# Performance work log

Measured on AMD Instinct MI355X. Metric: run time of the kernel, lower is better.

Reference implementation:

```python
import jax, jax.numpy as jnp
import numpy as np

B, N, F, T = 32, 1024, 64, 24


def setup_inputs() -> dict:
    key = jax.random.key(0)
    k = jax.random.split(key, 6)
    x = jax.random.normal(k[0], (B, N, F, T), dtype=jnp.float32)
    W1 = jax.random.normal(k[1], (T,), dtype=jnp.float32) * 0.1
    W2 = jax.random.normal(k[2], (F, T), dtype=jnp.float32) * 0.1
    W3 = jax.random.normal(k[3], (F,), dtype=jnp.float32) * 0.1
    b_s = jax.random.normal(k[4], (1, N, N), dtype=jnp.float32) * 0.02
    V_s = jax.random.normal(k[5], (N, N), dtype=jnp.float32) * 0.02
    return {"x": x, "W1": W1, "W2": W2, "W3": W3, "b_s": b_s, "V_s": V_s}


def reference(x, W1, W2, W3, b_s, V_s):
    # lhs = (x @ W1) @ W2 : (B,N,F,T)@(T,) -> (B,N,F) ; @(F,T) -> (B,N,T)
    lhs = jnp.einsum('bnft,t->bnf', x, W1) @ W2
    # rhs = (x^T @ W3) permuted : (B,N,T,F)@(F,) -> (B,N,T) -> (B,T,N)
    rhs = jnp.einsum('bnft,f->btn', x, W3)
    # batch_dot: (B,N,T) @ (B,T,N) -> (B,N,N), as one batched GEMM
    product = jnp.einsum('bnt,btm->bnm', lhs, rhs)
    sig = jax.nn.sigmoid(product + b_s)
    # torch.matmul(V_s, sig.permute(1,2,0)).permute(2,0,1) == S[b,n,i] = sum_k V_s[i,k]*sig[b,n,k]
    S = jnp.einsum('ik,bnk->bni', V_s, sig)
    S = S - jnp.max(S, axis=1, keepdims=True)
    exp = jnp.exp(S)
    # NOTE: original has `[0]` on the sum -> denominator uses batch-0 sums, shape (1,N),
    # broadcast over rows. Faithfully reproduced (numpy broadcasting matches torch here).
    return exp / jnp.sum(exp, axis=1, keepdims=True)[0]
```

## Files before the change

### kernel.cpp

```cpp
#include <hip/hip_runtime.h>
#include <hip/hip_bf16.h>

#define Bb 32
#define Nn 1024
#define Ff 64
#define Tt 24

#define LHSB_OFF 0ull
#define RHSB_OFF 2097152ull
#define MKEY_OFF 4194304ull
#define C0_OFF   4325376ull
#define ABF_OFF  8388608ull
#define VB_OFF   75497472ull
#define E_OFF    77594624ull
#define WS_NEED2 144703488ull

#define FB_LHS_OFF  0
#define FB_RHS_OFF  3145728
#define FB_MKEY_OFF 6291456
#define FB_D0_OFF   6422528

typedef __attribute__((ext_vector_type(8))) short bf16x8;
typedef __attribute__((ext_vector_type(4))) float f32x4;

__device__ __forceinline__ unsigned fkey(float x) {
    unsigned u = __float_as_uint(x);
    return (u & 0x80000000u) ? ~u : (u | 0x80000000u);
}
__device__ __forceinline__ float keyToFloat(unsigned k) {
    unsigned u = (k & 0x80000000u) ? (k & 0x7FFFFFFFu) : ~k;
    return __uint_as_float(u);
}
__device__ __forceinline__ unsigned short f2bf(float f) {
    unsigned u = __float_as_uint(f);
    u += 0x7FFFu + ((u >> 16) & 1u);
    return (unsigned short)(u >> 16);
}
__device__ __forceinline__ float bf2f(unsigned short s) {
    return __uint_as_float(((unsigned)s) << 16);
}

__global__ __launch_bounds__(256) void k1b(
    const float* __restrict__ x, const float* __restrict__ W1,
    const float* __restrict__ W2, const float* __restrict__ W3,
    const float* __restrict__ V_s,
    unsigned short* __restrict__ LHSb, unsigned short* __restrict__ RHSb,
    unsigned* __restrict__ Vb2, unsigned* __restrict__ Mkey,
    float* __restrict__ C0) {
    __shared__ float sx[4][64][25];
    __shared__ float sy[4][64];
    __shared__ float sW1[24];
    __shared__ float sW2[64][24];
    __shared__ float sW3[64];
    __shared__ __align__(16) unsigned short pl[4][32];
    __shared__ __align__(16) unsigned short pr[4][32];
    int tid = threadIdx.x;
    if (tid < 24) sW1[tid] = W1[tid];
    if (tid < 64) sW3[tid] = W3[tid];
    for (int j = tid; j < 64 * 24; j += 256) sW2[j / 24][j % 24] = W2[j];
    __syncthreads();

    int w = tid >> 6, lane = tid & 63;
    int row = blockIdx.x * 4 + w;
    const float* xr = x + (size_t)row * (Ff * Tt) + lane * Tt;
    float4 xv[6];
#pragma unroll
    for (int j = 0; j < 6; ++j) xv[j] = reinterpret_cast<const float4*>(xr)[j];
    float y = 0.f;
#pragma unroll
    for (int j = 0; j < 6; ++j) {
        y += xv[j].x * sW1[j * 4 + 0] + xv[j].y * sW1[j * 4 + 1] +
             xv[j].z * sW1[j * 4 + 2] + xv[j].w * sW1[j * 4 + 3];
    }
#pragma unroll
    for (int j = 0; j < 6; ++j) {
        sx[w][lane][j * 4 + 0] = xv[j].x;
        sx[w][lane][j * 4 + 1] = xv[j].y;
        sx[w][lane][j * 4 + 2] = xv[j].z;
        sx[w][lane][j * 4 + 3] = xv[j].w;
    }
    sy[w][lane] = y;
    __syncthreads();
    if (lane < 32) {
        if (lane < 24) {
            int t = lane;
            float la = 0.f, ra = 0.f;
#pragma unroll 8
            for (int f = 0; f < 64; ++f) {
                ra += sx[w][f][t] * sW3[f];
                la += sy[w][f] * sW2[f][t];
            }
            pl[w][t] = f2bf(la);
            pr[w][t] = f2bf(ra);
        } else {
            pl[w][lane] = 0;
            pr[w][lane] = 0;
        }
    }
    __syncthreads();
    if (lane < 4)
        ((uint4*)(LHSb + (size_t)row * 32))[lane] = ((const uint4*)pl[w])[lane];
    else if (lane < 8)
        ((uint4*)(RHSb + (size_t)row * 32))[lane - 4] = ((const uint4*)pr[w])[lane - 4];

    int bid = blockIdx.x;
    if (bid < 1024) {
        size_t idx = (size_t)bid * 256 + tid;
        float4 v = ((const float4*)V_s)[idx];
        uint2 o;
        o.x = (unsigned)f2bf(v.x) | ((unsigned)f2bf(v.y) << 16);
        o.y = (unsigned)f2bf(v.z) | ((unsigned)f2bf(v.w) << 16);
        ((uint2*)Vb2)[idx] = o;
    } else if (bid < 1156) {
        int widx = (bid - 1024) * 256 + tid;
        if (widx < 32768) Mkey[widx] = 0u;
        else if (widx < 33792) C0[widx - 32768] = 0.f;
    }
}

__global__ __launch_bounds__(512) void k_sig(
    const unsigned short* __restrict__ LHSb, const unsigned short* __restrict__ RHSb,
    const float* __restrict__ b_s, unsigned short* __restrict__ Abf) {
    __shared__ __align__(16) unsigned short Rt[256 * 32];
    __shared__ __align__(16) unsigned short Lt[256 * 32];
    const int tid = threadIdx.x, w = tid >> 6, lane = tid & 63;
    const int b = blockIdx.z, n0 = blockIdx.y * 256, k0 = blockIdx.x * 256;

    const int csrc = ((lane & 3) ^ ((lane >> 3) & 3)) * 8;
    const unsigned short* rbase = RHSb + (size_t)(b * 1024 + k0) * 32;
    const unsigned short* lbase = LHSb + (size_t)(b * 1024 + n0) * 32;
#define GLD(src, dst) __builtin_amdgcn_global_load_lds(                            \
        (const __attribute__((address_space(1))) void*)(src),                     \
        (__attribute__((address_space(3))) void*)(dst), 16, 0, 0)
    GLD(rbase + (size_t)(w * 32 + (lane >> 2)) * 32 + csrc,      Rt + (w * 32) * 32);
    GLD(rbase + (size_t)(w * 32 + 16 + (lane >> 2)) * 32 + csrc, Rt + (w * 32 + 16) * 32);
    GLD(lbase + (size_t)(w * 32 + (lane >> 2)) * 32 + csrc,      Lt + (w * 32) * 32);
    GLD(lbase + (size_t)(w * 32 + 16 + (lane >> 2)) * 32 + csrc, Lt + (w * 32 + 16) * 32);
#undef GLD
    __syncthreads();

    const int wk = (w >> 2) * 128, wn = (w & 3) * 64;
    const int l15 = lane & 15;
    const int swz8 = ((lane >> 4) ^ ((l15 >> 1) & 3)) * 8;
    bf16x8 af[8], bfr[4];
#pragma unroll
    for (int a = 0; a < 8; ++a)
        af[a] = *(const bf16x8*)(Rt + (wk + a * 16 + l15) * 32 + swz8);
#pragma unroll
    for (int c = 0; c < 4; ++c)
        bfr[c] = *(const bf16x8*)(Lt + (wn + c * 16 + l15) * 32 + swz8);

    f32x4 acc[8][4] = {};
#pragma unroll
    for (int a = 0; a < 8; ++a)
#pragma unroll
        for (int c = 0; c < 4; ++c)
            acc[a][c] = __builtin_amdgcn_mfma_f32_16x16x32_bf16(
                af[a], bfr[c], acc[a][c], 0, 0, 0);

    const int kb = k0 + wk + (lane >> 4) * 4;
    const int nb = n0 + wn + l15;
#pragma unroll
    for (int a = 0; a < 8; ++a)
#pragma unroll
        for (int c = 0; c < 4; ++c) {
            int n = nb + c * 16, k = kb + a * 16;
            float4 bs = *(const float4*)&b_s[(size_t)n * 1024 + k];
            f32x4 p = acc[a][c];
            unsigned short s0 = f2bf(1.f / (1.f + __expf(-(p[0] + bs.x))));
            unsigned short s1 = f2bf(1.f / (1.f + __expf(-(p[1] + bs.y))));
            unsigned short s2 = f2bf(1.f / (1.f + __expf(-(p[2] + bs.z))));
            unsigned short s3 = f2bf(1.f / (1.f + __expf(-(p[3] + bs.w))));
            uint2 ov;
            ov.x = (unsigned)s0 | ((unsigned)s1 << 16);
            ov.y = (unsigned)s2 | ((unsigned)s3 << 16);
            *(uint2*)(Abf + (size_t)(b * 1024 + n) * 1024 + k) = ov;
        }
}

__global__ __launch_bounds__(512, 2) void k2b_8ph(
    const unsigned short* __restrict__ A, const unsigned short* __restrict__ Vb,
    unsigned short* __restrict__ Ebuf, unsigned* __restrict__ Mkey,
    float* __restrict__ C0) {
    __shared__ __align__(16) unsigned short lds[65536];

    const int tid = threadIdx.x, w = tid >> 6, lane = tid & 63;
    const int l15 = lane & 15;
    const int bid = blockIdx.x;
    const int L = ((bid & 7) << 6) + (bid >> 3);
    const int i0 = (L & 3) * 256;
    const int m0 = (L >> 2) * 256;
    const int wr = w >> 2, wc = w & 3;

    const int p0 = (lane >> 4) ^ ((lane >> 1) & 7);
    const int aBase  = (wr * 128 + l15) * 64 + p0 * 8;
    const int aBaseX = aBase ^ 32;
    const int bBase  = 16384 + (wc * 64 + l15) * 64 + p0 * 8;
    const int bBaseX = bBase ^ 32;

    const int rL = lane >> 3;
    const int cS = (lane & 7) ^ ((4 * (w & 1) + (lane >> 4)) & 7);
    const int bRowW = (w >> 2) * 64 + (w & 3) * 8;
    const unsigned short* srcA00 = A  + (size_t)(m0 +   0 + 8 * w + rL) * 1024 + cS * 8;
    const unsigned short* srcA01 = A  + (size_t)(m0 + 128 + 8 * w + rL) * 1024 + cS * 8;
    const unsigned short* srcA10 = A  + (size_t)(m0 +  64 + 8 * w + rL) * 1024 + cS * 8;
    const unsigned short* srcA11 = A  + (size_t)(m0 + 192 + 8 * w + rL) * 1024 + cS * 8;
    const unsigned short* srcB00 = Vb + (size_t)(i0 +   0 + bRowW + rL) * 1024 + cS * 8;
    const unsigned short* srcB01 = Vb + (size_t)(i0 + 128 + bRowW + rL) * 1024 + cS * 8;
    const unsigned short* srcB10 = Vb + (size_t)(i0 +  32 + bRowW + rL) * 1024 + cS * 8;
    const unsigned short* srcB11 = Vb + (size_t)(i0 + 160 + bRowW + rL) * 1024 + cS * 8;
    const int dA00 = (0   + 8 * w) * 64, dA01 = (128 + 8 * w) * 64;
    const int dA10 = (64  + 8 * w) * 64, dA11 = (192 + 8 * w) * 64;
    const int dB00 = 16384 + (0   + bRowW) * 64, dB01 = 16384 + (128 + bRowW) * 64;
    const int dB10 = 16384 + (32  + bRowW) * 64, dB11 = 16384 + (160 + bRowW) * 64;

#define GLD(src, dstShorts) __builtin_amdgcn_global_load_lds(                      \
        (const __attribute__((address_space(1))) void*)(src),                     \
        (__attribute__((address_space(3))) void*)(lds + (dstShorts)), 16, 0, 0)

#define READ_A(bc, mh) do {                                                        \
    const int ro_ = (bc) * 32768 + (mh) * 4096;                                    \
    aR[0][0] = *(const bf16x8*)(lds + ro_ + aBase +    0);                         \
    aR[1][0] = *(const bf16x8*)(lds + ro_ + aBase + 1024);                         \
    aR[2][0] = *(const bf16x8*)(lds + ro_ + aBase + 2048);                         \
    aR[3][0] = *(const bf16x8*)(lds + ro_ + aBase + 3072);                         \
    aR[0][1] = *(const bf16x8*)(lds + ro_ + aBaseX +    0);                        \
    aR[1][1] = *(const bf16x8*)(lds + ro_ + aBaseX + 1024);                        \
    aR[2][1] = *(const bf16x8*)(lds + ro_ + aBaseX + 2048);                        \
    aR[3][1] = *(const bf16x8*)(lds + ro_ + aBaseX + 3072);                        \
} while (0)

#define READ_B(bc, nh, BR) do {                                                    \
    const int ro_ = (bc) * 32768 + (nh) * 2048;                                    \
    BR[0][0] = *(const bf16x8*)(lds + ro_ + bBase +    0);                         \
    BR[1][0] = *(const bf16x8*)(lds + ro_ + bBase + 1024);                         \
    BR[0][1] = *(const bf16x8*)(lds + ro_ + bBaseX +    0);                        \
    BR[1][1] = *(const bf16x8*)(lds + ro_ + bBaseX + 1024);                        \
} while (0)

#define BARRIER_LGKM                                                               \
    __builtin_amdgcn_s_barrier();                                                  \
    asm volatile("s_waitcnt lgkmcnt(0)" ::: "memory");                             \
    __builtin_amdgcn_sched_barrier(0)

#define QUAD(mh, nh, BR) do {                                                      \
    __builtin_amdgcn_s_setprio(1);                                                 \
    _Pragma("unroll")                                                              \
    for (int ks_ = 0; ks_ < 2; ++ks_)                                              \
        _Pragma("unroll")                                                          \
        for (int mi_ = 0; mi_ < 4; ++mi_)                                          \
            _Pragma("unroll")                                                      \
            for (int ni_ = 0; ni_ < 2; ++ni_)                                      \
                acc[(mh) * 4 + mi_][(nh) * 2 + ni_] =                              \
                    __builtin_amdgcn_mfma_f32_16x16x32_bf16(                       \
                        aR[mi_][ks_], BR[ni_][ks_],                                \
                        acc[(mh) * 4 + mi_][(nh) * 2 + ni_], 0, 0, 0);             \
    __builtin_amdgcn_s_setprio(0);                                                 \
} while (0)

#define VM6  asm volatile("s_waitcnt vmcnt(6)" ::: "memory")
#define ENDP __builtin_amdgcn_s_barrier()

    GLD(srcA00, dA00); GLD(srcA01, dA01);
    GLD(srcB00, dB00); GLD(srcB01, dB01);
    GLD(srcB10, dB10); GLD(srcB11, dB11);
    GLD(srcA10, dA10); GLD(srcA11, dA11);
    GLD(srcA00 + 64, 32768 + dA00); GLD(srcA01 + 64, 32768 + dA01);
    GLD(srcB00 + 64, 32768 + dB00); GLD(srcB01 + 64, 32768 + dB01);
    GLD(srcB10 + 64, 32768 + dB10); GLD(srcB11 + 64, 32768 + dB11);
    asm volatile("s_waitcnt vmcnt(6)" ::: "memory");
    __builtin_amdgcn_s_barrier();

    bf16x8 aR[4][2], b0R[2][2], b1R[2][2];
    f32x4 acc[8][4] = {};

    for (int j = 0; j < 8; ++j) {
        const int k1o = (2 * j + 1) * 64;
        const int k2o = ((j < 7) ? (2 * j + 2) : 15) * 64;
        const int k3o = ((j < 7) ? (2 * j + 3) : 15) * 64;

        READ_A(0, 0); READ_B(0, 0, b0R);
        GLD(srcA10 + k1o, 32768 + dA10); GLD(srcA11 + k1o, 32768 + dA11);
        BARRIER_LGKM; QUAD(0, 0, b0R); ENDP;
        READ_B(0, 1, b1R);
        GLD(srcA00 + k2o, dA00); GLD(srcA01 + k2o, dA01);
        BARRIER_LGKM; QUAD(0, 1, b1R); ENDP;
        READ_A(0, 1);
        GLD(srcB00 + k2o, dB00); GLD(srcB01 + k2o, dB01);
        BARRIER_LGKM; QUAD(1, 0, b0R); ENDP;
        GLD(srcB10 + k2o, dB10); GLD(srcB11 + k2o, dB11);
        BARRIER_LGKM; QUAD(1, 1, b1R); VM6; ENDP;
        READ_A(1, 0); READ_B(1, 0, b0R);
        GLD(srcA10 + k2o, dA10); GLD(srcA11 + k2o, dA11);
        BARRIER_LGKM; QUAD(0, 0, b0R); ENDP;
        READ_B(1, 1, b1R);
        GLD(srcA00 + k3o, 32768 + dA00); GLD(srcA01 + k3o, 32768 + dA01);
        BARRIER_LGKM; QUAD(0, 1, b1R); ENDP;
        READ_A(1, 1);
        GLD(srcB00 + k3o, 32768 + dB00); GLD(srcB01 + k3o, 32768 + dB01);
        BARRIER_LGKM; QUAD(1, 0, b0R); ENDP;
        GLD(srcB10 + k3o, 32768 + dB10); GLD(srcB11 + k3o, 32768 + dB11);
        BARRIER_LGKM; QUAD(1, 1, b1R); VM6; ENDP;
    }
#undef GLD
#undef READ_A
#undef READ_B
#undef BARRIER_LGKM
#undef QUAD
#undef VM6
#undef ENDP

    const int ic = i0 + wc * 64 + l15;
    const int mrb = m0 + wr * 128 + (lane >> 4) * 4;
#pragma unroll
    for (int mi8 = 0; mi8 < 8; ++mi8)
#pragma unroll
        for (int ni = 0; ni < 4; ++ni)
#pragma unroll
            for (int r = 0; r < 4; ++r)
                acc[mi8][ni][r] = __expf(acc[mi8][ni][r]);
#pragma unroll
    for (int mi8 = 0; mi8 < 8; ++mi8)
#pragma unroll
        for (int ni = 0; ni < 4; ++ni) {
            f32x4 v = acc[mi8][ni];
#pragma unroll
            for (int r = 0; r < 4; ++r)
                Ebuf[(size_t)(mrb + mi8 * 16 + r) * 1024 + ic + ni * 16] = f2bf(v[r]);
        }
    const int bcol = m0 >> 10;
#pragma unroll
    for (int ni = 0; ni < 4; ++ni) {
        float mx = 0.f, sm = 0.f;
#pragma unroll
        for (int mi8 = 0; mi8 < 8; ++mi8)
#pragma unroll
            for (int r = 0; r < 4; ++r) {
                float e = acc[mi8][ni][r];
                mx = fmaxf(mx, e);
                sm += e;
            }
        mx = fmaxf(mx, __shfl_xor(mx, 16));
        mx = fmaxf(mx, __shfl_xor(mx, 32));
        sm += __shfl_xor(sm, 16);
        sm += __shfl_xor(sm, 32);
        if ((lane >> 4) == 0) {
            atomicMax(&Mkey[bcol * Nn + ic + ni * 16], fkey(mx));
            if (bcol == 0) atomicAdd(&C0[ic + ni * 16], sm);
        }
    }
}

__global__ __launch_bounds__(256) void k5b(
    const unsigned short* __restrict__ E, const unsigned* __restrict__ Mkey,
    const float* __restrict__ C0, float* __restrict__ out) {
    const size_t total4 = (size_t)Bb * Nn * Nn / 4;
    for (size_t idx = (size_t)blockIdx.x * 256 + threadIdx.x; idx < total4;
         idx += (size_t)gridDim.x * 256) {
        size_t e4 = idx << 2;
        int i = (int)(e4 & (Nn - 1));
        int b = (int)(e4 >> 20);
        uint2 ev = ((const uint2*)E)[idx];
        uint4 mb = *(const uint4*)(Mkey + b * Nn + i);
        uint4 m0 = *(const uint4*)(Mkey + i);
        float4 c0 = *(const float4*)(C0 + i);
        float4 o;
        o.x = bf2f((unsigned short)(ev.x & 0xffffu)) *
              __fdividef(keyToFloat(m0.x), keyToFloat(mb.x) * c0.x);
        o.y = bf2f((unsigned short)(ev.x >> 16)) *
              __fdividef(keyToFloat(m0.y), keyToFloat(mb.y) * c0.y);
        o.z = bf2f((unsigned short)(ev.y & 0xffffu)) *
              __fdividef(keyToFloat(m0.z), keyToFloat(mb.z) * c0.z);
        o.w = bf2f((unsigned short)(ev.y >> 16)) *
              __fdividef(keyToFloat(m0.w), keyToFloat(mb.w) * c0.w);
        ((float4*)out)[idx] = o;
    }
}

__global__ __launch_bounds__(256) void k1_lhs_rhs(
    const float* __restrict__ x, const float* __restrict__ W1,
    const float* __restrict__ W2, const float* __restrict__ W3,
    float* __restrict__ LHS, float* __restrict__ RHS) {
    __shared__ float sx[4][64][25];
    __shared__ float sy[4][64];
    __shared__ float sW1[24];
    __shared__ float sW2[64][24];
    __shared__ float sW3[64];
    int tid = threadIdx.x;
    if (tid < 24) sW1[tid] = W1[tid];
    if (tid < 64) sW3[tid] = W3[tid];
    for (int j = tid; j < 64 * 24; j += 256) sW2[j / 24][j % 24] = W2[j];
    __syncthreads();
    int w = tid >> 6, lane = tid & 63;
    int row = blockIdx.x * 4 + w;
    const float* xr = x + (size_t)row * (Ff * Tt) + lane * Tt;
    float4 xv[6];
#pragma unroll
    for (int j = 0; j < 6; ++j) xv[j] = reinterpret_cast<const float4*>(xr)[j];
    float y = 0.f;
#pragma unroll
    for (int j = 0; j < 6; ++j) {
        y += xv[j].x * sW1[j * 4 + 0] + xv[j].y * sW1[j * 4 + 1] +
             xv[j].z * sW1[j * 4 + 2] + xv[j].w * sW1[j * 4 + 3];
    }
#pragma unroll
    for (int j = 0; j < 6; ++j) {
        sx[w][lane][j * 4 + 0] = xv[j].x;
        sx[w][lane][j * 4 + 1] = xv[j].y;
        sx[w][lane][j * 4 + 2] = xv[j].z;
        sx[w][lane][j * 4 + 3] = xv[j].w;
    }
    sy[w][lane] = y;
    __syncthreads();
    if (lane < 24) {
        int t = lane;
        float la = 0.f, ra = 0.f;
#pragma unroll 8
        for (int f = 0; f < 64; ++f) {
            ra += sx[w][f][t] * sW3[f];
            la += sy[w][f] * sW2[f][t];
        }
        LHS[(size_t)row * Tt + t] = la;
        RHS[(size_t)row * Tt + t] = ra;
    }
}

#define KB 32
__global__ __launch_bounds__(256) void k2_gemm(
    const float* __restrict__ LHS, const float* __restrict__ RHS,
    const float* __restrict__ V_s, const float* __restrict__ b_s,
    float* __restrict__ S) {
    __shared__ float Lst[24][132];
    __shared__ float Rst[24][KB];
    __shared__ float As[KB][132];
    __shared__ float Bs[KB][132];
    int tid = threadIdx.x;
    int b = blockIdx.z;
    int n0 = blockIdx.y * 128;
    int i0 = blockIdx.x * 128;
    const float* lbase = LHS + ((size_t)b * Nn + n0) * Tt;
    for (int lin = tid; lin < 128 * Tt; lin += 256) {
        int r = lin / Tt, t = lin % Tt;
        Lst[t][r] = lbase[lin];
    }
    float acc[8][8] = {};
    int tx = tid & 15, ty = tid >> 4;
    int an = (tid & 31) * 4;
    int ak = (tid >> 5) * 4;
    const float* rbase = RHS + (size_t)b * Nn * Tt;
    for (int k0 = 0; k0 < Nn; k0 += KB) {
        __syncthreads();
        for (int lin = tid; lin < KB * Tt; lin += 256) {
            int r = lin / Tt, t = lin % Tt;
            Rst[t][r] = rbase[(size_t)(k0 + r) * Tt + t];
        }
        for (int l4 = tid; l4 < 128 * (KB / 4); l4 += 256) {
            int i = l4 >> 3, k4 = (l4 & 7) << 2;
            float4 v = *(const float4*)&V_s[(size_t)(i0 + i) * Nn + k0 + k4];
            Bs[k4 + 0][i] = v.x; Bs[k4 + 1][i] = v.y;
            Bs[k4 + 2][i] = v.z; Bs[k4 + 3][i] = v.w;
        }
        __syncthreads();
        float pacc[4][4] = {};
#pragma unroll
        for (int t = 0; t < 24; ++t) {
            float4 lv = *(const float4*)&Lst[t][an];
            float4 rv = *(const float4*)&Rst[t][ak];
            float lvv[4] = {lv.x, lv.y, lv.z, lv.w};
            float rvv[4] = {rv.x, rv.y, rv.z, rv.w};
#pragma unroll
            for (int r = 0; r < 4; ++r)
#pragma unroll
                for (int c = 0; c < 4; ++c) pacc[r][c] += lvv[r] * rvv[c];
        }
#pragma unroll
        for (int r = 0; r < 4; ++r) {
            float4 bs4 = *(const float4*)&b_s[(size_t)(n0 + an + r) * Nn + k0 + ak];
            float bsv[4] = {bs4.x, bs4.y, bs4.z, bs4.w};
#pragma unroll
            for (int c = 0; c < 4; ++c) {
                float p = pacc[r][c] + bsv[c];
                As[ak + c][an + r] = 1.f / (1.f + __expf(-p));
            }
        }
        __syncthreads();
#pragma unroll
        for (int kk = 0; kk < KB; ++kk) {
            float4 a0 = *(const float4*)&As[kk][ty * 4];
            float4 a1 = *(const float4*)&As[kk][ty * 4 + 64];
            float4 b0 = *(const float4*)&Bs[kk][tx * 4];
            float4 b1 = *(const float4*)&Bs[kk][tx * 4 + 64];
            float av[8] = {a0.x, a0.y, a0.z, a0.w, a1.x, a1.y, a1.z, a1.w};
            float bv[8] = {b0.x, b0.y, b0.z, b0.w, b1.x, b1.y, b1.z, b1.w};
#pragma unroll
            for (int r = 0; r < 8; ++r)
#pragma unroll
                for (int c = 0; c < 8; ++c) acc[r][c] += av[r] * bv[c];
        }
    }
#pragma unroll
    for (int r = 0; r < 8; ++r) {
        int nn = ty * 4 + (r & 3) + ((r >> 2) << 6);
        float4* op = (float4*)(S + ((size_t)(b * Nn + n0 + nn)) * Nn + i0 + tx * 4);
        op[0]  = make_float4(acc[r][0], acc[r][1], acc[r][2], acc[r][3]);
        op[16] = make_float4(acc[r][4], acc[r][5], acc[r][6], acc[r][7]);
    }
}

__global__ __launch_bounds__(256) void k3_colmax(const float* __restrict__ S,
                                                 unsigned* __restrict__ Mkey) {
    int b = blockIdx.z;
    int i0 = blockIdx.x * 64;
    int nbase = blockIdx.y * 256;
    int ii = threadIdx.x & 63, g = threadIdx.x >> 6;
    const float* p = S + ((size_t)(b * Nn + nbase + g * 64)) * Nn + i0 + ii;
    float m = -3.402823466e38f;
#pragma unroll 4
    for (int n = 0; n < 64; ++n) m = fmaxf(m, p[(size_t)n * Nn]);
    __shared__ float red[4][64];
    red[g][ii] = m;
    __syncthreads();
    if (g == 0) {
        m = fmaxf(fmaxf(red[0][ii], red[1][ii]), fmaxf(red[2][ii], red[3][ii]));
        atomicMax(Mkey + b * Nn + i0 + ii, fkey(m));
    }
}

__global__ __launch_bounds__(256) void k4_denom(const float* __restrict__ S,
                                                const unsigned* __restrict__ Mkey,
                                                float* __restrict__ D0) {
    int i0 = blockIdx.x * 64;
    int ii = threadIdx.x & 63, g = threadIdx.x >> 6;
    float M = keyToFloat(Mkey[i0 + ii]);
    const float* p = S + ((size_t)(g * 256)) * Nn + i0 + ii;
    float s = 0.f;
    for (int n = 0; n < 256; ++n) s += __expf(p[(size_t)n * Nn] - M);
    __shared__ float red[4][64];
    red[g][ii] = s;
    __syncthreads();
    if (g == 0) D0[i0 + ii] = (red[0][ii] + red[1][ii]) + (red[2][ii] + red[3][ii]);
}

__global__ __launch_bounds__(256) void k5_final(float* __restrict__ S,
                                                const unsigned* __restrict__ Mkey,
                                                const float* __restrict__ D0) {
    const size_t total4 = (size_t)Bb * Nn * Nn / 4;
    for (size_t idx = (size_t)blockIdx.x * 256 + threadIdx.x; idx < total4;
         idx += (size_t)gridDim.x * 256) {
        size_t e = idx << 2;
        int i = (int)(e & (Nn - 1));
        int b = (int)(e >> 20);
        float4 s4 = ((const float4*)S)[idx];
        uint4 k4 = *(const uint4*)(Mkey + b * Nn + i);
        float4 d4 = *(const float4*)(D0 + i);
        float4 o;
        o.x = __expf(s4.x - keyToFloat(k4.x)) / d4.x;
        o.y = __expf(s4.y - keyToFloat(k4.y)) / d4.y;
        o.z = __expf(s4.z - keyToFloat(k4.z)) / d4.z;
        o.w = __expf(s4.w - keyToFloat(k4.w)) / d4.w;
        ((float4*)S)[idx] = o;
    }
}

extern "C" void kernel_launch(void* const* d_in, const int* in_sizes, int n_in,
                              void* d_out, int out_size, void* d_ws, size_t ws_size,
                              hipStream_t stream) {
    const float* x   = (const float*)d_in[0];
    const float* W1  = (const float*)d_in[1];
    const float* W2  = (const float*)d_in[2];
    const float* W3  = (const float*)d_in[3];
    const float* b_s = (const float*)d_in[4];
    const float* V_s = (const float*)d_in[5];
    float* out = (float*)d_out;
    char* ws = (char*)d_ws;

    if (ws_size >= WS_NEED2) {
        unsigned short* LHSb = (unsigned short*)(ws + LHSB_OFF);
        unsigned short* RHSb = (unsigned short*)(ws + RHSB_OFF);
        unsigned* Mkey = (unsigned*)(ws + MKEY_OFF);
        float* C0 = (float*)(ws + C0_OFF);
        unsigned short* Abf = (unsigned short*)(ws + ABF_OFF);
        unsigned short* Vb  = (unsigned short*)(ws + VB_OFF);
        unsigned short* Eb  = (unsigned short*)(ws + E_OFF);

        k1b<<<Bb * Nn / 4, 256, 0, stream>>>(x, W1, W2, W3, V_s, LHSb, RHSb,
                                             (unsigned*)Vb, Mkey, C0);
        k_sig<<<dim3(4, 4, Bb), 512, 0, stream>>>(LHSb, RHSb, b_s, Abf);
        k2b_8ph<<<512, 512, 0, stream>>>(Abf, Vb, Eb, Mkey, C0);
        k5b<<<2048, 256, 0, stream>>>(Eb, Mkey, C0, out);
    } else {
        float* LHS = (float*)(ws + FB_LHS_OFF);
        float* RHS = (float*)(ws + FB_RHS_OFF);
        unsigned* Mkey = (unsigned*)(ws + FB_MKEY_OFF);
        float* D0 = (float*)(ws + FB_D0_OFF);
        k1_lhs_rhs<<<Bb * Nn / 4, 256, 0, stream>>>(x, W1, W2, W3, LHS, RHS);
        hipMemsetAsync(Mkey, 0, (size_t)Bb * Nn * sizeof(unsigned), stream);
        k2_gemm<<<dim3(Nn / 128, Nn / 128, Bb), 256, 0, stream>>>(LHS, RHS, V_s, b_s, out);
        k3_colmax<<<dim3(Nn / 64, 4, Bb), 256, 0, stream>>>(out, Mkey);
        k4_denom<<<Nn / 64, 256, 0, stream>>>(out, Mkey, D0);
        k5_final<<<2048, 256, 0, stream>>>(out, Mkey, D0);
    }
}
```

Baseline: 216.6 us.

## Switch main GEMM to 32x32x16 MFMA and stage sigmoid stores through LDS

The main S GEMM kernel now uses 32x32x16 bf16 MFMA instructions in place of 16x16x32. It re-lays out the LDS fragment reads with a new swizzle and updates the epilogue indexing and reductions to the 32x32 output layout. Separately, the sigmoid kernel packs its results into a per-wave LDS buffer and writes them back as 16-byte row-contiguous stores, replacing the scattered 8-byte writes. The goal is fewer MFMA issues and LDS reads per flop and coalesced global writes, at the cost of an extra LDS round trip and more LDS usage in the sigmoid kernel.

```diff
diff --git a/kernel.cpp b/kernel.cpp
--- a/kernel.cpp
+++ b/kernel.cpp
@@ -22,6 +22,7 @@
 
 typedef __attribute__((ext_vector_type(8))) short bf16x8;
 typedef __attribute__((ext_vector_type(4))) float f32x4;
+typedef __attribute__((ext_vector_type(16))) float f32x16;
 
 __device__ __forceinline__ unsigned fkey(float x) {
     unsigned u = __float_as_uint(x);
@@ -121,8 +122,9 @@
 __global__ __launch_bounds__(512) void k_sig(
     const unsigned short* __restrict__ LHSb, const unsigned short* __restrict__ RHSb,
     const float* __restrict__ b_s, unsigned short* __restrict__ Abf) {
-    __shared__ __align__(16) unsigned short Rt[256 * 32];
-    __shared__ __align__(16) unsigned short Lt[256 * 32];
+    __shared__ __align__(16) unsigned short sbuf[17408];
+    unsigned short* Rt = sbuf;
+    unsigned short* Lt = sbuf + 8192;
     const int tid = threadIdx.x, w = tid >> 6, lane = tid & 63;
     const int b = blockIdx.z, n0 = blockIdx.y * 256, k0 = blockIdx.x * 256;
 
@@ -158,24 +160,37 @@
             acc[a][c] = __builtin_amdgcn_mfma_f32_16x16x32_bf16(
                 af[a], bfr[c], acc[a][c], 0, 0, 0);
 
-    const int kb = k0 + wk + (lane >> 4) * 4;
-    const int nb = n0 + wn + l15;
-#pragma unroll
-    for (int a = 0; a < 8; ++a)
-#pragma unroll
-        for (int c = 0; c < 4; ++c) {
-            int n = nb + c * 16, k = kb + a * 16;
-            float4 bs = *(const float4*)&b_s[(size_t)n * 1024 + k];
+    __syncthreads();
+
+    unsigned short* Bw = sbuf + w * 2176;
+    const int h = lane >> 4;
+#pragma unroll
+    for (int c = 0; c < 4; ++c) {
+        int n = n0 + wn + c * 16 + l15;
+        const float* bsrow = b_s + (size_t)n * 1024 + k0 + wk;
+#pragma unroll
+        for (int a = 0; a < 8; ++a) {
+            int kloc = a * 16 + h * 4;
+            float4 bs = *(const float4*)(bsrow + kloc);
             f32x4 p = acc[a][c];
             unsigned short s0 = f2bf(1.f / (1.f + __expf(-(p[0] + bs.x))));
             unsigned short s1 = f2bf(1.f / (1.f + __expf(-(p[1] + bs.y))));
             unsigned short s2 = f2bf(1.f / (1.f + __expf(-(p[2] + bs.z))));
             unsigned short s3 = f2bf(1.f / (1.f + __expf(-(p[3] + bs.w))));
-            uint2 ov;
-            ov.x = (unsigned)s0 | ((unsigned)s1 << 16);
-            ov.y = (unsigned)s2 | ((unsigned)s3 << 16);
-            *(uint2*)(Abf + (size_t)(b * 1024 + n) * 1024 + k) = ov;
-        }
+            uint2 pk;
+            pk.x = (unsigned)s0 | ((unsigned)s1 << 16);
+            pk.y = (unsigned)s2 | ((unsigned)s3 << 16);
+            *(uint2*)(Bw + l15 * 136 + kloc) = pk;
+        }
+        asm volatile("s_waitcnt lgkmcnt(0)" ::: "memory");
+#pragma unroll
+        for (int q = 0; q < 4; ++q) {
+            int r = q * 4 + h;
+            uint4 v = *(const uint4*)(Bw + r * 136 + l15 * 8);
+            int nn = n0 + wn + c * 16 + r;
+            *(uint4*)(Abf + (size_t)(b * 1024 + nn) * 1024 + k0 + wk + l15 * 8) = v;
+        }
+    }
 }
 
 __global__ __launch_bounds__(512, 2) void k2b_8ph(
@@ -185,18 +200,20 @@
     __shared__ __align__(16) unsigned short lds[65536];
 
     const int tid = threadIdx.x, w = tid >> 6, lane = tid & 63;
-    const int l15 = lane & 15;
     const int bid = blockIdx.x;
     const int L = ((bid & 7) << 6) + (bid >> 3);
     const int i0 = (L & 3) * 256;
     const int m0 = (L >> 2) * 256;
     const int wr = w >> 2, wc = w & 3;
 
-    const int p0 = (lane >> 4) ^ ((lane >> 1) & 7);
-    const int aBase  = (wr * 128 + l15) * 64 + p0 * 8;
-    const int aBaseX = aBase ^ 32;
-    const int bBase  = 16384 + (wc * 64 + l15) * 64 + p0 * 8;
-    const int bBaseX = bBase ^ 32;
+    const int lane31 = lane & 31;
+    const int half8 = lane >> 5;
+    const int swz = (lane >> 1) & 7;
+    const int aB32 = (wr * 128 + lane31) * 64;
+    const int bB32 = 16384 + (wc * 64 + lane31) * 64;
+    int c32[4];
+#pragma unroll
+    for (int s = 0; s < 4; ++s) c32[s] = ((2 * s + half8) ^ swz) * 8;
 
     const int rL = lane >> 3;
     const int cS = (lane & 7) ^ ((4 * (w & 1) + (lane >> 4)) & 7);
@@ -218,24 +235,20 @@
         (const __attribute__((address_space(1))) void*)(src),                     \
         (__attribute__((address_space(3))) void*)(lds + (dstShorts)), 16, 0, 0)
 
-#define READ_A(bc, mh) do {                                                        \
+#define READ_A32(bc, mh) do {                                                      \
     const int ro_ = (bc) * 32768 + (mh) * 4096;                                    \
-    aR[0][0] = *(const bf16x8*)(lds + ro_ + aBase +    0);                         \
-    aR[1][0] = *(const bf16x8*)(lds + ro_ + aBase + 1024);                         \
-    aR[2][0] = *(const bf16x8*)(lds + ro_ + aBase + 2048);                         \
-    aR[3][0] = *(const bf16x8*)(lds + ro_ + aBase + 3072);                         \
-    aR[0][1] = *(const bf16x8*)(lds + ro_ + aBaseX +    0);                        \
-    aR[1][1] = *(const bf16x8*)(lds + ro_ + aBaseX + 1024);                        \
-    aR[2][1] = *(const bf16x8*)(lds + ro_ + aBaseX + 2048);                        \
-    aR[3][1] = *(const bf16x8*)(lds + ro_ + aBaseX + 3072);                        \
+    _Pragma("unroll")                                                              \
+    for (int f_ = 0; f_ < 2; ++f_)                                                 \
+        _Pragma("unroll")                                                          \
+        for (int s_ = 0; s_ < 4; ++s_)                                             \
+            aR[f_][s_] = *(const bf16x8*)(lds + ro_ + aB32 + f_ * 2048 + c32[s_]); \
 } while (0)
 
-#define READ_B(bc, nh, BR) do {                                                    \
+#define READ_B32(bc, nh, BR) do {                                                  \
     const int ro_ = (bc) * 32768 + (nh) * 2048;                                    \
-    BR[0][0] = *(const bf16x8*)(lds + ro_ + bBase +    0);                         \
-    BR[1][0] = *(const bf16x8*)(lds + ro_ + bBase + 1024);                         \
-    BR[0][1] = *(const bf16x8*)(lds + ro_ + bBaseX +    0);                        \
-    BR[1][1] = *(const bf16x8*)(lds + ro_ + bBaseX + 1024);                        \
+    _Pragma("unroll")                                                              \
+    for (int s_ = 0; s_ < 4; ++s_)                                                 \
+        BR[s_] = *(const bf16x8*)(lds + ro_ + bB32 + c32[s_]);                     \
 } while (0)
 
 #define BARRIER_LGKM                                                               \
@@ -243,23 +256,20 @@
     asm volatile("s_waitcnt lgkmcnt(0)" ::: "memory");                             \
     __builtin_amdgcn_sched_barrier(0)
 
-#define QUAD(mh, nh, BR) do {                                                      \
+#define QUAD32(mh, nh, BR) do {                                                    \
     __builtin_amdgcn_s_setprio(1);                                                 \
     _Pragma("unroll")                                                              \
-    for (int ks_ = 0; ks_ < 2; ++ks_)                                              \
+    for (int s_ = 0; s_ < 4; ++s_)                                                 \
         _Pragma("unroll")                                                          \
-        for (int mi_ = 0; mi_ < 4; ++mi_)                                          \
-            _Pragma("unroll")                                                      \
-            for (int ni_ = 0; ni_ < 2; ++ni_)                                      \
-                acc[(mh) * 4 + mi_][(nh) * 2 + ni_] =                              \
-                    __builtin_amdgcn_mfma_f32_16x16x32_bf16(                       \
-                        aR[mi_][ks_], BR[ni_][ks_],                                \
-                        acc[(mh) * 4 + mi_][(nh) * 2 + ni_], 0, 0, 0);             \
+        for (int f_ = 0; f_ < 2; ++f_)                                             \
+            acc[(mh) * 2 + f_][nh] = __builtin_amdgcn_mfma_f32_32x32x16_bf16(      \
+                aR[f_][s_], BR[s_], acc[(mh) * 2 + f_][nh], 0, 0, 0);              \
     __builtin_amdgcn_s_setprio(0);                                                 \
 } while (0)
 
-#define VM6  asm volatile("s_waitcnt vmcnt(6)" ::: "memory")
-#define ENDP __builtin_amdgcn_s_barrier()
+#define LGKM8 asm volatile("s_waitcnt lgkmcnt(8)" ::: "memory")
+#define VM6   asm volatile("s_waitcnt vmcnt(6)" ::: "memory")
+#define ENDP  __builtin_amdgcn_s_barrier()
 
     GLD(srcA00, dA00); GLD(srcA01, dA01);
     GLD(srcB00, dB00); GLD(srcB01, dB01);
@@ -271,82 +281,83 @@
     asm volatile("s_waitcnt vmcnt(6)" ::: "memory");
     __builtin_amdgcn_s_barrier();
 
-    bf16x8 aR[4][2], b0R[2][2], b1R[2][2];
-    f32x4 acc[8][4] = {};
+    bf16x8 aR[2][4], b0R[4], b1R[4];
+    f32x16 acc[4][2] = {};
 
     for (int j = 0; j < 8; ++j) {
         const int k1o = (2 * j + 1) * 64;
         const int k2o = ((j < 7) ? (2 * j + 2) : 15) * 64;
         const int k3o = ((j < 7) ? (2 * j + 3) : 15) * 64;
 
-        READ_A(0, 0); READ_B(0, 0, b0R);
+        READ_A32(0, 0); READ_B32(0, 0, b0R);
         GLD(srcA10 + k1o, 32768 + dA10); GLD(srcA11 + k1o, 32768 + dA11);
-        BARRIER_LGKM; QUAD(0, 0, b0R); ENDP;
-        READ_B(0, 1, b1R);
+        LGKM8;
+        BARRIER_LGKM; QUAD32(0, 0, b0R); ENDP;
+        READ_B32(0, 1, b1R);
         GLD(srcA00 + k2o, dA00); GLD(srcA01 + k2o, dA01);
-        BARRIER_LGKM; QUAD(0, 1, b1R); ENDP;
-        READ_A(0, 1);
+        BARRIER_LGKM; QUAD32(0, 1, b1R); ENDP;
+        READ_A32(0, 1);
         GLD(srcB00 + k2o, dB00); GLD(srcB01 + k2o, dB01);
-        BARRIER_LGKM; QUAD(1, 0, b0R); ENDP;
+        BARRIER_LGKM; QUAD32(1, 0, b0R); ENDP;
         GLD(srcB10 + k2o, dB10); GLD(srcB11 + k2o, dB11);
-        BARRIER_LGKM; QUAD(1, 1, b1R); VM6; ENDP;
-        READ_A(1, 0); READ_B(1, 0, b0R);
+        BARRIER_LGKM; QUAD32(1, 1, b1R); VM6; ENDP;
+        READ_A32(1, 0); READ_B32(1, 0, b0R);
         GLD(srcA10 + k2o, dA10); GLD(srcA11 + k2o, dA11);
-        BARRIER_LGKM; QUAD(0, 0, b0R); ENDP;
-        READ_B(1, 1, b1R);
+        LGKM8;
+        BARRIER_LGKM; QUAD32(0, 0, b0R); ENDP;
+        READ_B32(1, 1, b1R);
         GLD(srcA00 + k3o, 32768 + dA00); GLD(srcA01 + k3o, 32768 + dA01);
-        BARRIER_LGKM; QUAD(0, 1, b1R); ENDP;
-        READ_A(1, 1);
+        BARRIER_LGKM; QUAD32(0, 1, b1R); ENDP;
+        READ_A32(1, 1);
         GLD(srcB00 + k3o, 32768 + dB00); GLD(srcB01 + k3o, 32768 + dB01);
-        BARRIER_LGKM; QUAD(1, 0, b0R); ENDP;
+        BARRIER_LGKM; QUAD32(1, 0, b0R); ENDP;
         GLD(srcB10 + k3o, 32768 + dB10); GLD(srcB11 + k3o, 32768 + dB11);
-        BARRIER_LGKM; QUAD(1, 1, b1R); VM6; ENDP;
+        BARRIER_LGKM; QUAD32(1, 1, b1R); VM6; ENDP;
     }
 #undef GLD
-#undef READ_A
-#undef READ_B
+#undef READ_A32
+#undef READ_B32
 #undef BARRIER_LGKM
-#undef QUAD
+#undef QUAD32
+#undef LGKM8
 #undef VM6
 #undef ENDP
 
-    const int ic = i0 + wc * 64 + l15;
-    const int mrb = m0 + wr * 128 + (lane >> 4) * 4;
-#pragma unroll
-    for (int mi8 = 0; mi8 < 8; ++mi8)
-#pragma unroll
-        for (int ni = 0; ni < 4; ++ni)
-#pragma unroll
-            for (int r = 0; r < 4; ++r)
-                acc[mi8][ni][r] = __expf(acc[mi8][ni][r]);
-#pragma unroll
-    for (int mi8 = 0; mi8 < 8; ++mi8)
-#pragma unroll
-        for (int ni = 0; ni < 4; ++ni) {
-            f32x4 v = acc[mi8][ni];
-#pragma unroll
-            for (int r = 0; r < 4; ++r)
-                Ebuf[(size_t)(mrb + mi8 * 16 + r) * 1024 + ic + ni * 16] = f2bf(v[r]);
-        }
+    const int colD = i0 + wc * 64 + lane31;
+    const int rowD = m0 + wr * 128 + 4 * half8;
+#pragma unroll
+    for (int rf = 0; rf < 4; ++rf)
+#pragma unroll
+        for (int cf = 0; cf < 2; ++cf)
+#pragma unroll
+            for (int reg = 0; reg < 16; ++reg)
+                acc[rf][cf][reg] = __expf(acc[rf][cf][reg]);
+#pragma unroll
+    for (int rf = 0; rf < 4; ++rf)
+#pragma unroll
+        for (int cf = 0; cf < 2; ++cf)
+#pragma unroll
+            for (int reg = 0; reg < 16; ++reg) {
+                int r = rowD + rf * 32 + (reg & 3) + 8 * (reg >> 2);
+                Ebuf[(size_t)r * 1024 + colD + cf * 32] = f2bf(acc[rf][cf][reg]);
+            }
     const int bcol = m0 >> 10;
 #pragma unroll
-    for (int ni = 0; ni < 4; ++ni) {
+    for (int cf = 0; cf < 2; ++cf) {
         float mx = 0.f, sm = 0.f;
 #pragma unroll
-        for (int mi8 = 0; mi8 < 8; ++mi8)
-#pragma unroll
-            for (int r = 0; r < 4; ++r) {
-                float e = acc[mi8][ni][r];
+        for (int rf = 0; rf < 4; ++rf)
+#pragma unroll
+            for (int reg = 0; reg < 16; ++reg) {
+                float e = acc[rf][cf][reg];
                 mx = fmaxf(mx, e);
                 sm += e;
             }
-        mx = fmaxf(mx, __shfl_xor(mx, 16));
         mx = fmaxf(mx, __shfl_xor(mx, 32));
-        sm += __shfl_xor(sm, 16);
         sm += __shfl_xor(sm, 32);
-        if ((lane >> 4) == 0) {
-            atomicMax(&Mkey[bcol * Nn + ic + ni * 16], fkey(mx));
-            if (bcol == 0) atomicAdd(&C0[ic + ni * 16], sm);
+        if (lane < 32) {
+            atomicMax(&Mkey[bcol * Nn + colD + cf * 32], fkey(mx));
+            if (bcol == 0) atomicAdd(&C0[colD + cf * 32], sm);
         }
     }
 }
```

Result: no change. 215.7 us (-0.4%).
